# Performance work log

Measured on AMD Instinct MI355X. Metric: run time of the kernel, lower is better.

## Reference

```python
import jax, jax.numpy as jnp
import numpy as np

K = 3  # kernel_size
P = 1  # padding (must satisfy K == 2*P+1 for the original einsum to be shape-valid)


def setup_inputs() -> dict:
    key = jax.random.key(0)
    k1, k2, k3 = jax.random.split(key, 3)
    b, i, c, L, o = 16, 64, 4, 4096, 64
    x = jax.random.normal(k1, (b, i, c, L), dtype=jnp.float32)
    time_tensor = jax.random.uniform(k2, (b, c, L), dtype=jnp.float32)
    weights = jax.random.normal(k3, (o, i, c, K), dtype=jnp.float32)
    return {"x": x, "time_tensor": time_tensor, "weights": weights}


def reference(x, time_tensor, weights):
    """x: (b,i,c,L), time_tensor: (b,c,L), weights: (o,i,c,K) -> (b,o,c,L).

    Faithful to the torch module: pad x/time by P on the time axis, unfold x
    into sliding windows, pad the unfolded tensor again by P, multiply by the
    time scalar per (b,c,l) and contract over (i,k), then crop P from each end.
    The time factor is scalar per output element, so we factor it out of the
    einsum instead of materializing the (b,o,i,c,k,l) dynamic_weights tensor --
    mathematically identical, massively cheaper.
    """
    xp = jnp.pad(x, ((0, 0), (0, 0), (0, 0), (P, P)))            # (b,i,c,L+2P)
    tp = jnp.pad(time_tensor, ((0, 0), (0, 0), (P, P)))          # (b,c,L+2P)
    Lw = xp.shape[-1] - K + 1                                    # == L since K=2P+1
    # unfold -> (b,i,c,K,Lw), matching torch's permute(0,2,1,4,3) after transpose
    xu = jnp.stack([xp[..., j:j + Lw] for j in range(K)], axis=-2)
    xu = jnp.transpose(xu, (0, 2, 1, 3, 4))                      # (b,c,i,K,Lw)
    xu = jnp.pad(xu, ((0, 0), (0, 0), (0, 0), (0, 0), (P, P)))   # (b,c,i,K,Lw+2P)
    conv = jnp.einsum('oick,bcikl->bocl', weights, xu)           # (b,o,c,L+2P)
    out = conv * tp[:, None, :, :]
    return out[..., P:-P]                                        # (b,o,c,L)
```

## Files before the change

kernel.cpp:

```cpp
#include <hip/hip_runtime.h>


#define NB 16
#define NI 64
#define NC 4
#define NL 4096
#define NO 64
#define KW 3
#define LT 32
#define NCH 8
#define LBLK (LT * NCH)
#define ROWS (LBLK + 2)
#define ROWB 128
#define LDSB (ROWS * ROWB)

#define W_PACK_BYTES (NO * NI * NC * KW * 2)

typedef float f32x4 __attribute__((ext_vector_type(4)));
typedef short bf16x8 __attribute__((ext_vector_type(8)));

__device__ inline unsigned short f2bf(float f) {
    unsigned int u = __builtin_bit_cast(unsigned int, f);
    u += 0x7FFFu + ((u >> 16) & 1u);
    return (unsigned short)(u >> 16);
}

__device__ __forceinline__ void block_sync_lds() {
    asm volatile("s_waitcnt lgkmcnt(0)" ::: "memory");
    __builtin_amdgcn_s_barrier();
    asm volatile("" ::: "memory");
}

__global__ __launch_bounds__(256)
void prepack_w_kernel(const float* __restrict__ w, unsigned short* __restrict__ wp) {
    const int idx = blockIdx.x * 256 + threadIdx.x;
    const float v = w[idx];
    const int k = idx % 3;
    int r = idx / 3;
    const int c = r & 3;  r >>= 2;
    const int i = r & 63;
    const int o = r >> 6;
    const int cc   = k * 2 + (i >> 5);
    const int lane = (((i >> 3) & 3) << 4) | (o & 15);
    const int j    = i & 7;
    const int wv   = o >> 4;
    wp[(((c * 4 + wv) * 6 + cc) * 64 + lane) * 8 + j] = f2bf(v);
}

__device__ __forceinline__ void stage_load(const float* __restrict__ xb,
                                           int l0q, int g2, f32x4 s[2]) {
    const float* p = xb + (size_t)(2 * g2) * (NC * NL) + l0q;
    s[0] = *(const f32x4*)(p);
    s[1] = *(const f32x4*)(p + NC * NL);
}

__device__ __forceinline__ void stage_write(char* __restrict__ lds,
                                            int ch, int q, int g2,
                                            const f32x4 s[2]) {
#pragma unroll
    for (int r = 0; r < 4; ++r) {
        const int row = ch * LT + 4 * q + r + 1;
        const unsigned int pk =
            (unsigned int)f2bf(s[0][r]) | ((unsigned int)f2bf(s[1][r]) << 16);
        *(unsigned int*)(lds + row * ROWB + ((4 * g2) ^ ((row & 7) << 4))) = pk;
    }
}

__device__ __forceinline__ void compute_chunk(const char* __restrict__ lds,
                                              const bf16x8 wfrag[6],
                                              const float* __restrict__ tb,
                                              float* __restrict__ ob,
                                              int ch, int lb0, int lane) {
    const int lcol  = lane & 15;
    const int ksub2 = (lane >> 4) * 16;
#pragma unroll
    for (int lt = 0; lt < 2; ++lt) {
        const int l0 = lb0 + ch * LT + lt * 16 + (lane >> 4) * 4;
        const f32x4 tv = *(const f32x4*)(tb + l0);
        f32x4 acc = {};
#pragma unroll
        for (int cc = 0; cc < 6; ++cc) {
            const int row = ch * LT + lt * 16 + lcol + (cc >> 1);
            const int off = row * ROWB + ((((cc & 1) << 6) + ksub2) ^ ((row & 7) << 4));
            const bf16x8 xf = *(const bf16x8*)(lds + off);
            acc = __builtin_amdgcn_mfma_f32_16x16x32_bf16(xf, wfrag[cc], acc, 0, 0, 0);
        }
        f32x4 r;
#pragma unroll
        for (int qq = 0; qq < 4; ++qq) r[qq] = acc[qq] * tv[qq];
        *(f32x4*)(ob + l0) = r;
    }
}

__global__ __launch_bounds__(256, 4)
void tconv_mfma_kernel(const float* __restrict__ x,
                       const float* __restrict__ tt,
                       const unsigned short* __restrict__ wp,
                       float* __restrict__ out)
{
    __shared__ char lds[LDSB];

    const int t    = threadIdx.x;
    const int lane = t & 63;
    const int wave = t >> 6;
    const int c    = blockIdx.y;
    const int b    = blockIdx.z;
    const int lb0  = blockIdx.x * LBLK;
    const int g2   = t >> 3;
    const int q    = t & 7;
    const int lq   = 4 * q;

    const float* xb = x + ((size_t)b * NI * NC + c) * NL;
    const float* tb = tt + (size_t)(b * NC + c) * NL;
    float* ob = out + ((size_t)b * NO * NC
                       + (size_t)(wave * 16 + (lane & 15)) * NC + c) * NL;

    f32x4 sA[2], sB[2];
    stage_load(xb, lb0 + 0 * LT + lq, g2, sA);
    stage_load(xb, lb0 + 1 * LT + lq, g2, sB);
    float h = 0.f; int hrow = 0, hcol = 0;
    if (t < 128) {
        const int which = t & 1;
        const int i     = t >> 1;
        hrow = which ? (LBLK + 1) : 0;
        hcol = 2 * i;
        const int lh = which ? (lb0 + LBLK) : (lb0 - 1);
        if (lh >= 0 && lh < NL) h = xb[(size_t)i * (NC * NL) + lh];
    }

    bf16x8 wfrag[6];
    {
        const bf16x8* wpb = (const bf16x8*)wp + (size_t)((c * 4 + wave) * 6) * 64 + lane;
#pragma unroll
        for (int cc = 0; cc < 6; ++cc) wfrag[cc] = wpb[cc * 64];
    }

    stage_write(lds, 0, q, g2, sA);
    stage_write(lds, 1, q, g2, sB);
    if (t < 128)
        *(unsigned short*)(lds + hrow * ROWB + (hcol ^ ((hrow & 7) << 4))) = f2bf(h);
    block_sync_lds();

#pragma unroll
    for (int cn = 0; cn < NCH - 2; ++cn) {
        if ((cn & 1) == 0) {
            stage_load(xb, lb0 + (cn + 2) * LT + lq, g2, sA);
            compute_chunk(lds, wfrag, tb, ob, cn, lb0, lane);
            stage_write(lds, cn + 2, q, g2, sA);
        } else {
            stage_load(xb, lb0 + (cn + 2) * LT + lq, g2, sB);
            compute_chunk(lds, wfrag, tb, ob, cn, lb0, lane);
            stage_write(lds, cn + 2, q, g2, sB);
        }
        block_sync_lds();
    }

    compute_chunk(lds, wfrag, tb, ob, NCH - 2, lb0, lane);
    compute_chunk(lds, wfrag, tb, ob, NCH - 1, lb0, lane);
}

extern "C" void kernel_launch(void* const* d_in, const int* in_sizes, int n_in,
                              void* d_out, int out_size, void* d_ws, size_t ws_size,
                              hipStream_t stream) {
    const float* x  = (const float*)d_in[0];
    const float* tt = (const float*)d_in[1];
    const float* w  = (const float*)d_in[2];
    float* out = (float*)d_out;
    unsigned short* wpck = (unsigned short*)d_ws;

    prepack_w_kernel<<<dim3(NO * NI * NC * KW / 256), dim3(256), 0, stream>>>(w, wpck);

    dim3 grid(NL / LBLK, NC, NB);
    tconv_mfma_kernel<<<grid, dim3(256), 0, stream>>>(x, tt, wpck, out);
}
```

Baseline: 33.01 us.

## Remap waves to 32 outputs by 16 positions so each x fragment feeds two MFMAs

Each wave now covers two 16-wide output-channel groups and one half of the 32-position chunk, where before it covered one output group and both halves. Every LDS x fragment read is reused for two MFMAs, which halves LDS read traffic per MFMA and gives two independent accumulator chains. In exchange each wave holds twice as many weight fragments in registers, adding register pressure at the 4-blocks-per-CU launch bound. Output stores now come from two channel groups rather than two position tiles.

```diff
diff --git a/kernel.cpp b/kernel.cpp
--- a/kernel.cpp
+++ b/kernel.cpp
@@ -67,29 +67,30 @@
 }
 
 __device__ __forceinline__ void compute_chunk(const char* __restrict__ lds,
-                                              const bf16x8 wfrag[6],
+                                              const bf16x8 wfrag[2][6],
                                               const float* __restrict__ tb,
-                                              float* __restrict__ ob,
-                                              int ch, int lb0, int lane) {
+                                              float* __restrict__ ob0,
+                                              float* __restrict__ ob1,
+                                              int ch, int lb0, int lane, int lh) {
     const int lcol  = lane & 15;
     const int ksub2 = (lane >> 4) * 16;
+    const int l0 = lb0 + ch * LT + lh * 16 + (lane >> 4) * 4;
+    const f32x4 tv = *(const f32x4*)(tb + l0);
+
+    f32x4 acc0 = {}, acc1 = {};
 #pragma unroll
-    for (int lt = 0; lt < 2; ++lt) {
-        const int l0 = lb0 + ch * LT + lt * 16 + (lane >> 4) * 4;
-        const f32x4 tv = *(const f32x4*)(tb + l0);
-        f32x4 acc = {};
+    for (int cc = 0; cc < 6; ++cc) {
+        const int row = ch * LT + lh * 16 + lcol + (cc >> 1);
+        const int off = row * ROWB + ((((cc & 1) << 6) + ksub2) ^ ((row & 7) << 4));
+        const bf16x8 xf = *(const bf16x8*)(lds + off);
+        acc0 = __builtin_amdgcn_mfma_f32_16x16x32_bf16(xf, wfrag[0][cc], acc0, 0, 0, 0);
+        acc1 = __builtin_amdgcn_mfma_f32_16x16x32_bf16(xf, wfrag[1][cc], acc1, 0, 0, 0);
+    }
+    f32x4 r0, r1;
 #pragma unroll
-        for (int cc = 0; cc < 6; ++cc) {
-            const int row = ch * LT + lt * 16 + lcol + (cc >> 1);
-            const int off = row * ROWB + ((((cc & 1) << 6) + ksub2) ^ ((row & 7) << 4));
-            const bf16x8 xf = *(const bf16x8*)(lds + off);
-            acc = __builtin_amdgcn_mfma_f32_16x16x32_bf16(xf, wfrag[cc], acc, 0, 0, 0);
-        }
-        f32x4 r;
-#pragma unroll
-        for (int qq = 0; qq < 4; ++qq) r[qq] = acc[qq] * tv[qq];
-        *(f32x4*)(ob + l0) = r;
-    }
+    for (int qq = 0; qq < 4; ++qq) { r0[qq] = acc0[qq] * tv[qq]; r1[qq] = acc1[qq] * tv[qq]; }
+    *(f32x4*)(ob0 + l0) = r0;
+    *(f32x4*)(ob1 + l0) = r1;
 }
 
 __global__ __launch_bounds__(256, 4)
@@ -103,6 +104,8 @@
     const int t    = threadIdx.x;
     const int lane = t & 63;
     const int wave = t >> 6;
+    const int oh   = wave >> 1;
+    const int lh   = wave & 1;
     const int c    = blockIdx.y;
     const int b    = blockIdx.z;
     const int lb0  = blockIdx.x * LBLK;
@@ -112,8 +115,9 @@
 
     const float* xb = x + ((size_t)b * NI * NC + c) * NL;
     const float* tb = tt + (size_t)(b * NC + c) * NL;
-    float* ob = out + ((size_t)b * NO * NC
-                       + (size_t)(wave * 16 + (lane & 15)) * NC + c) * NL;
+    float* ob0 = out + ((size_t)b * NO * NC
+                        + (size_t)(oh * 32 + (lane & 15)) * NC + c) * NL;
+    float* ob1 = ob0 + (size_t)16 * NC * NL;
 
     f32x4 sA[2], sB[2];
     stage_load(xb, lb0 + 0 * LT + lq, g2, sA);
@@ -124,15 +128,18 @@
         const int i     = t >> 1;
         hrow = which ? (LBLK + 1) : 0;
         hcol = 2 * i;
-        const int lh = which ? (lb0 + LBLK) : (lb0 - 1);
-        if (lh >= 0 && lh < NL) h = xb[(size_t)i * (NC * NL) + lh];
+        const int lhh = which ? (lb0 + LBLK) : (lb0 - 1);
+        if (lhh >= 0 && lhh < NL) h = xb[(size_t)i * (NC * NL) + lhh];
     }
 
-    bf16x8 wfrag[6];
+    bf16x8 wfrag[2][6];
     {
-        const bf16x8* wpb = (const bf16x8*)wp + (size_t)((c * 4 + wave) * 6) * 64 + lane;
+        const bf16x8* wpb = (const bf16x8*)wp + (size_t)((c * 4 + oh * 2) * 6) * 64 + lane;
 #pragma unroll
-        for (int cc = 0; cc < 6; ++cc) wfrag[cc] = wpb[cc * 64];
+        for (int s = 0; s < 2; ++s)
+#pragma unroll
+            for (int cc = 0; cc < 6; ++cc)
+                wfrag[s][cc] = wpb[(s * 6 + cc) * 64];
     }
 
     stage_write(lds, 0, q, g2, sA);
@@ -145,18 +152,18 @@
     for (int cn = 0; cn < NCH - 2; ++cn) {
         if ((cn & 1) == 0) {
             stage_load(xb, lb0 + (cn + 2) * LT + lq, g2, sA);
-            compute_chunk(lds, wfrag, tb, ob, cn, lb0, lane);
+            compute_chunk(lds, wfrag, tb, ob0, ob1, cn, lb0, lane, lh);
             stage_write(lds, cn + 2, q, g2, sA);
         } else {
             stage_load(xb, lb0 + (cn + 2) * LT + lq, g2, sB);
-            compute_chunk(lds, wfrag, tb, ob, cn, lb0, lane);
+            compute_chunk(lds, wfrag, tb, ob0, ob1, cn, lb0, lane, lh);
             stage_write(lds, cn + 2, q, g2, sB);
         }
         block_sync_lds();
     }
 
-    compute_chunk(lds, wfrag, tb, ob, NCH - 2, lb0, lane);
-    compute_chunk(lds, wfrag, tb, ob, NCH - 1, lb0, lane);
+    compute_chunk(lds, wfrag, tb, ob0, ob1, NCH - 2, lb0, lane, lh);
+    compute_chunk(lds, wfrag, tb, ob0, ob1, NCH - 1, lb0, lane, lh);
 }
 
 extern "C" void kernel_launch(void* const* d_in, const int* in_sizes, int n_in,
```

Result: no change. 33.46 us (+1.4%).
